# Performance work log

Measured on AMD Instinct MI355X. Metric: run time of the kernel, lower is better.

Reference implementation:

```python
import jax, jax.numpy as jnp
import numpy as np

D_IN, D_HID, D_CLS, N_CLASSES = 1024, 256, 128, 4
CELL_IN = 512
N = 50000


def setup_inputs() -> dict:
    key = jax.random.key(0)
    ks = jax.random.split(key, 20)
    s = 0.02
    inp = {
        "x_path": jax.random.normal(ks[0], (1, N, D_IN), jnp.float32),
        "x_cell": jax.random.normal(ks[1], (1, N, CELL_IN), jnp.float32),
        # wsi_net / cell_net projections
        "wsi_w": jax.random.normal(ks[2], (D_IN, D_HID), jnp.float32) * s,
        "wsi_b": jnp.zeros((D_HID,), jnp.float32),
        "cell_w": jax.random.normal(ks[3], (CELL_IN, D_HID), jnp.float32) * s,
        "cell_b": jnp.zeros((D_HID,), jnp.float32),
        # cross-attention Q/K/V
        "wq_w": jax.random.normal(ks[4], (D_HID, D_HID), jnp.float32) * s,
        "wq_b": jnp.zeros((D_HID,), jnp.float32),
        "wk_w": jax.random.normal(ks[5], (D_HID, D_HID), jnp.float32) * s,
        "wk_b": jnp.zeros((D_HID,), jnp.float32),
        "wv_w": jax.random.normal(ks[6], (D_HID, D_HID), jnp.float32) * s,
        "wv_b": jnp.zeros((D_HID,), jnp.float32),
        # gated attention (L=D=256, n_classes=1)
        "aa_w": jax.random.normal(ks[7], (D_HID, D_HID), jnp.float32) * s,
        "aa_b": jnp.zeros((D_HID,), jnp.float32),
        "ab_w": jax.random.normal(ks[8], (D_HID, D_HID), jnp.float32) * s,
        "ab_b": jnp.zeros((D_HID,), jnp.float32),
        "ac_w": jax.random.normal(ks[9], (D_HID, 1), jnp.float32) * s,
        "ac_b": jnp.zeros((1,), jnp.float32),
        # classifier MLP
        "c1_w": jax.random.normal(ks[10], (D_HID, D_CLS), jnp.float32) * s,
        "c1_b": jnp.zeros((D_CLS,), jnp.float32),
        "c2_w": jax.random.normal(ks[11], (D_CLS, N_CLASSES), jnp.float32) * s,
        "c2_b": jnp.zeros((N_CLASSES,), jnp.float32),
    }
    return inp


def reference(x_path, x_cell, wsi_w, wsi_b, cell_w, cell_b,
              wq_w, wq_b, wk_w, wk_b, wv_w, wv_b,
              aa_w, aa_b, ab_w, ab_b, ac_w, ac_b,
              c1_w, c1_b, c2_w, c2_b):
    xp = x_path[0]            # (N, D_IN)
    xc = x_cell[0]            # (N, CELL_IN)
    # instance-level projections (dropout inactive at eval)
    h_path = jax.nn.relu(xp @ wsi_w + wsi_b)    # (N, d)
    h_cell = jax.nn.relu(xc @ cell_w + cell_b)  # (N, d)
    # cross attention with per-instance seq_len=1 (bmm over N singleton batches)
    q = h_cell @ wq_w + wq_b
    k = h_path @ wk_w + wk_b
    v = h_path @ wv_w + wv_b
    scores = (jnp.einsum('nd,nd->n', q, k) / jnp.sqrt(jnp.float32(q.shape[-1])))[:, None, None]  # (N,1,1)
    attn_w = jax.nn.softmax(scores, axis=-1)     # (N,1,1), trivially ones
    fused = attn_w[:, 0, :] * v                  # (N, d)
    # gated attention MIL pooling
    a = jnp.tanh(fused @ aa_w + aa_b)
    b = jax.nn.sigmoid(fused @ ab_w + ab_b)
    A = (a * b) @ ac_w + ac_b                    # (N, 1)
    A_t = A.T                                    # (1, N)
    pooled = jax.nn.softmax(A_t, axis=1) @ fused # (1, d)
    # classifier MLP
    risk = jax.nn.relu(pooled @ c1_w + c1_b) @ c2_w + c2_b  # (1, n_classes)
    return risk
```

## Files before the change

kernel.cpp:

```cpp
#include <hip/hip_runtime.h>
#include <hip/hip_bf16.h>
#include <math.h>

#define D_IN 1024
#define D_HID 256
#define D_CLS 128
#define N_CLASSES 4
#define N_INST 50000

#define NPAD 50176
#define TILES 392
#define RG2 128
#define GB (NPAD / RG2)
#define PSTR 258
#define NEG_BIG (-1e30f)

#define ROWS 64
#define NBLK ((N_INST + ROWS - 1) / ROWS)
#define NB2 64
#define CHUNK ((NBLK + NB2 - 1) / NB2)

#define WS_W1T   0u
#define WS_WVT   524288u
#define WS_WAT   655360u
#define WS_WBT   786432u
#define WS_CNT   917504u
#define WS_P1    917760u
#define WS_XT    1322304u
#define WS_H     (WS_XT + 102760448u)
#define WS_NEED2 ((size_t)WS_H + 25690112u)
#define WS_P1F   917504u
#define WS_P2F   1724800u

typedef __attribute__((ext_vector_type(8))) short bf16x8;
typedef __attribute__((ext_vector_type(4))) float f32x4;

__device__ __forceinline__ short f2bf(float x) {
    __hip_bfloat16 h = __float2bfloat16(x);
    return *reinterpret_cast<short*>(&h);
}
__device__ __forceinline__ float fast_tanh(float x) {
    float e = __expf(2.f * x);
    return 1.f - 2.f * __builtin_amdgcn_rcpf(e + 1.f);
}
__device__ __forceinline__ float fast_sigmoid(float x) {
    return __builtin_amdgcn_rcpf(1.f + __expf(-x));
}
__device__ __forceinline__ bf16x8 cvt8(float4 a, float4 b) {
    bf16x8 r;
    r[0] = f2bf(a.x); r[1] = f2bf(a.y); r[2] = f2bf(a.z); r[3] = f2bf(a.w);
    r[4] = f2bf(b.x); r[5] = f2bf(b.y); r[6] = f2bf(b.z); r[7] = f2bf(b.w);
    return r;
}
__device__ __forceinline__ bf16x8 load_cvt8(const float* __restrict__ p) {
    return cvt8(*(const float4*)p, *(const float4*)(p + 4));
}

__global__ void convert_weights(const float* __restrict__ w1, const float* __restrict__ wv,
                                const float* __restrict__ wa, const float* __restrict__ wb,
                                __hip_bfloat16* __restrict__ w1t, __hip_bfloat16* __restrict__ wvt,
                                __hip_bfloat16* __restrict__ wat, __hip_bfloat16* __restrict__ wbt) {
    __shared__ __hip_bfloat16 T[64][68];
    int b = blockIdx.x, tid = threadIdx.x;
    const float* src; __hip_bfloat16* dst; int K, tr, tc;
    if (b < 64) { src = w1; dst = w1t; K = D_IN; tr = b >> 2; tc = b & 3; }
    else {
        int m = (b - 64) >> 4, t = (b - 64) & 15;
        src = (m == 0) ? wv : (m == 1) ? wa : wb;
        dst = (m == 0) ? wvt : (m == 1) ? wat : wbt;
        K = D_HID; tr = t >> 2; tc = t & 3;
    }
    int k0 = tr * 64, n0 = tc * 64;
#pragma unroll
    for (int p = 0; p < 4; p++) {
        int lin = p * 256 + tid;
        int r = lin >> 4;
        int c4 = (lin & 15) << 2;
        float4 v = *(const float4*)(src + (size_t)(k0 + r) * D_HID + n0 + c4);
        T[c4 + 0][r] = __float2bfloat16(v.x);
        T[c4 + 1][r] = __float2bfloat16(v.y);
        T[c4 + 2][r] = __float2bfloat16(v.z);
        T[c4 + 3][r] = __float2bfloat16(v.w);
    }
    __syncthreads();
#pragma unroll
    for (int p = 0; p < 4; p++) {
        int lin = p * 256 + tid;
        int n = lin >> 4;
        int kq = (lin & 15) << 2;
        ushort4 o;
        o.x = *(unsigned short*)&T[n][kq + 0];
        o.y = *(unsigned short*)&T[n][kq + 1];
        o.z = *(unsigned short*)&T[n][kq + 2];
        o.w = *(unsigned short*)&T[n][kq + 3];
        *(ushort4*)(dst + (size_t)(n0 + n) * K + k0 + kq) = o;
    }
}

__global__ __launch_bounds__(256, 2) void convert_xt(const float* __restrict__ xp,
                                                     __hip_bfloat16* __restrict__ xt) {
    __shared__ __hip_bfloat16 T[128][264];
    const int t = blockIdx.x >> 2;
    const int g = blockIdx.x & 3;
    const int tid = threadIdx.x;
    const int row = tid >> 1;
    const int half = tid & 1;
    const int row_g = t * 128 + row;
    const bool valid = row_g < N_INST;
    const float* src = xp + (size_t)row_g * D_IN + g * 256 + half * 128;
#pragma unroll 4
    for (int j = 0; j < 32; j++) {
        float4 v = {0.f, 0.f, 0.f, 0.f};
        if (valid) v = *(const float4*)(src + j * 4);
        int c = half * 128 + j * 4;
        ushort4 o;
        o.x = (unsigned short)f2bf(v.x);
        o.y = (unsigned short)f2bf(v.y);
        o.z = (unsigned short)f2bf(v.z);
        o.w = (unsigned short)f2bf(v.w);
        *(ushort4*)&T[row][c] = o;
    }
    __syncthreads();
#pragma unroll
    for (int i = 0; i < 16; i++) {
        int s = i * 256 + tid;
        int kg = s >> 7;
        int r2 = s & 127;
        bf16x8 v = *(const bf16x8*)&T[r2][kg * 8];
        int chunk = g * 8 + (kg >> 2);
        int quad = kg & 3;
        *(bf16x8*)(xt + (((size_t)(t * 32 + chunk) * 4 + quad) << 10) + r2 * 8) = v;
    }
}

__global__ __launch_bounds__(256, 2) void mcat_stage1(const __hip_bfloat16* __restrict__ xt,
                                                      const __hip_bfloat16* __restrict__ w1t,
                                                      const float* __restrict__ b1,
                                                      __hip_bfloat16* __restrict__ hout) {
    const int t    = blockIdx.x;
    const int tid  = threadIdx.x;
    const int wave = tid >> 6;
    const int lane = tid & 63;
    const int quad = lane >> 4;
    const int l16  = lane & 15;

    f32x4 acc[8][4];
    f32x4 zero = {0.f, 0.f, 0.f, 0.f};
#pragma unroll
    for (int i = 0; i < 8; i++)
#pragma unroll
        for (int j = 0; j < 4; j++) acc[i][j] = zero;

    const __hip_bfloat16* abase = xt + (size_t)t * 131072 + quad * 1024 + l16 * 8;
    const __hip_bfloat16* wbase[4];
#pragma unroll
    for (int ct = 0; ct < 4; ct++)
        wbase[ct] = w1t + (size_t)(wave * 64 + ct * 16 + l16) * D_IN + quad * 8;

#pragma unroll 4
    for (int kc = 0; kc < 32; kc++) {
        bf16x8 af[8];
#pragma unroll
        for (int rt = 0; rt < 8; rt++)
            af[rt] = *(const bf16x8*)(abase + kc * 4096 + rt * 128);
        bf16x8 bf[4];
#pragma unroll
        for (int ct = 0; ct < 4; ct++)
            bf[ct] = *(const bf16x8*)(wbase[ct] + kc * 32);
#pragma unroll
        for (int ct = 0; ct < 4; ct++)
#pragma unroll
            for (int rt = 0; rt < 8; rt++)
                acc[rt][ct] = __builtin_amdgcn_mfma_f32_16x16x32_bf16(af[rt], bf[ct], acc[rt][ct], 0, 0, 0);
    }

#pragma unroll
    for (int ct = 0; ct < 4; ct++) {
        const int col = wave * 64 + ct * 16 + l16;
        const float bias = b1[col];
        __hip_bfloat16* hb = hout + (((size_t)(t * 8 + (col >> 5)) * 4 + ((col >> 3) & 3)) << 10) + (col & 7);
#pragma unroll
        for (int rt = 0; rt < 8; rt++)
#pragma unroll
            for (int r = 0; r < 4; r++) {
                int row = rt * 16 + quad * 4 + r;
                hb[row * 8] = __float2bfloat16(fmaxf(acc[rt][ct][r] + bias, 0.f));
            }
    }
}

__global__ __launch_bounds__(512, 1) void mcat_stage2(const __hip_bfloat16* __restrict__ h,
                          const __hip_bfloat16* __restrict__ wvt, const float* __restrict__ bv,
                          const __hip_bfloat16* __restrict__ wat, const float* __restrict__ ba,
                          const __hip_bfloat16* __restrict__ wbt, const float* __restrict__ bb,
                          const float* __restrict__ acw, const float* __restrict__ acb,
                          float* __restrict__ p1, unsigned int* __restrict__ counter,
                          const float* __restrict__ c1w, const float* __restrict__ c1b,
                          const float* __restrict__ c2w, const float* __restrict__ c2b,
                          float* __restrict__ out) {
    __shared__ __hip_bfloat16 Vs[RG2][264];
    __shared__ float Apart[8][RG2];
    __shared__ float ExpW[RG2];
    __shared__ float smx[4];
    __shared__ float scb[GB];
    __shared__ float pooled[D_HID];
    __shared__ float r1v[D_CLS];

    const int tid  = threadIdx.x;
    const int wave = tid >> 6;
    const int lane = tid & 63;
    const int quad = lane >> 4;
    const int l16  = lane & 15;
    const int cb   = wave * 32;
    const int row0 = blockIdx.x * RG2;

    f32x4 acc[8][2];
    f32x4 zero = {0.f, 0.f, 0.f, 0.f};

    const __hip_bfloat16* hb = h + (size_t)blockIdx.x * 32768 + quad * 1024 + l16 * 8;
#pragma unroll
    for (int i = 0; i < 8; i++) { acc[i][0] = zero; acc[i][1] = zero; }
    {
        const __hip_bfloat16* w0 = wvt + (size_t)(cb + l16) * D_HID + quad * 8;
        const __hip_bfloat16* w1p = w0 + 16 * D_HID;
#pragma unroll
        for (int ks = 0; ks < 8; ks++) {
            bf16x8 b0 = *(const bf16x8*)(w0 + ks * 32);
            bf16x8 b1f = *(const bf16x8*)(w1p + ks * 32);
#pragma unroll
            for (int rt = 0; rt < 8; rt++) {
                bf16x8 af = *(const bf16x8*)(hb + ks * 4096 + rt * 128);
                acc[rt][0] = __builtin_amdgcn_mfma_f32_16x16x32_bf16(af, b0, acc[rt][0], 0, 0, 0);
                acc[rt][1] = __builtin_amdgcn_mfma_f32_16x16x32_bf16(af, b1f, acc[rt][1], 0, 0, 0);
            }
        }
    }
#pragma unroll
    for (int ct = 0; ct < 2; ct++) {
        int col = cb + ct * 16 + l16;
        float bias = bv[col];
#pragma unroll
        for (int rt = 0; rt < 8; rt++)
#pragma unroll
            for (int r = 0; r < 4; r++)
                Vs[rt * 16 + quad * 4 + r][col] = __float2bfloat16(acc[rt][ct][r] + bias);
    }
    __syncthreads();

    float a_reg[8][2][4];
#pragma unroll
    for (int i = 0; i < 8; i++) { acc[i][0] = zero; acc[i][1] = zero; }
    {
        const __hip_bfloat16* w0 = wat + (size_t)(cb + l16) * D_HID + quad * 8;
        const __hip_bfloat16* w1p = w0 + 16 * D_HID;
#pragma unroll
        for (int ks = 0; ks < 8; ks++) {
            bf16x8 b0 = *(const bf16x8*)(w0 + ks * 32);
            bf16x8 b1f = *(const bf16x8*)(w1p + ks * 32);
#pragma unroll
            for (int rt = 0; rt < 8; rt++) {
                bf16x8 af = *(const bf16x8*)&Vs[rt * 16 + l16][ks * 32 + quad * 8];
                acc[rt][0] = __builtin_amdgcn_mfma_f32_16x16x32_bf16(af, b0, acc[rt][0], 0, 0, 0);
                acc[rt][1] = __builtin_amdgcn_mfma_f32_16x16x32_bf16(af, b1f, acc[rt][1], 0, 0, 0);
            }
        }
    }
#pragma unroll
    for (int ct = 0; ct < 2; ct++) {
        float bias = ba[cb + ct * 16 + l16];
#pragma unroll
        for (int rt = 0; rt < 8; rt++)
#pragma unroll
            for (int r = 0; r < 4; r++)
                a_reg[rt][ct][r] = fast_tanh(acc[rt][ct][r] + bias);
    }

#pragma unroll
    for (int i = 0; i < 8; i++) { acc[i][0] = zero; acc[i][1] = zero; }
    {
        const __hip_bfloat16* w0 = wbt + (size_t)(cb + l16) * D_HID + quad * 8;
        const __hip_bfloat16* w1p = w0 + 16 * D_HID;
#pragma unroll
        for (int ks = 0; ks < 8; ks++) {
            bf16x8 b0 = *(const bf16x8*)(w0 + ks * 32);
            bf16x8 b1f = *(const bf16x8*)(w1p + ks * 32);
#pragma unroll
            for (int rt = 0; rt < 8; rt++) {
                bf16x8 af = *(const bf16x8*)&Vs[rt * 16 + l16][ks * 32 + quad * 8];
                acc[rt][0] = __builtin_amdgcn_mfma_f32_16x16x32_bf16(af, b0, acc[rt][0], 0, 0, 0);
                acc[rt][1] = __builtin_amdgcn_mfma_f32_16x16x32_bf16(af, b1f, acc[rt][1], 0, 0, 0);
            }
        }
    }
    {
        float acw0 = acw[cb + l16], acw1 = acw[cb + 16 + l16];
        float bb0 = bb[cb + l16],  bb1 = bb[cb + 16 + l16];
        float sp[8][4];
#pragma unroll
        for (int rt = 0; rt < 8; rt++)
#pragma unroll
            for (int r = 0; r < 4; r++) {
                float g0 = a_reg[rt][0][r] * fast_sigmoid(acc[rt][0][r] + bb0);
                float g1 = a_reg[rt][1][r] * fast_sigmoid(acc[rt][1][r] + bb1);
                sp[rt][r] = g0 * acw0 + g1 * acw1;
            }
#pragma unroll
        for (int off = 1; off < 16; off <<= 1)
#pragma unroll
            for (int rt = 0; rt < 8; rt++)
#pragma unroll
                for (int r = 0; r < 4; r++)
                    sp[rt][r] += __shfl_xor(sp[rt][r], off, 16);
        if (l16 == 0) {
#pragma unroll
            for (int rt = 0; rt < 8; rt++)
#pragma unroll
                for (int r = 0; r < 4; r++)
                    Apart[wave][rt * 16 + quad * 4 + r] = sp[rt][r];
        }
    }
    __syncthreads();

    if (tid < 64) {
        float A0 = acb[0], A1 = acb[0];
#pragma unroll
        for (int w = 0; w < 8; w++) { A0 += Apart[w][tid]; A1 += Apart[w][tid + 64]; }
        bool v0 = (row0 + tid) < N_INST;
        bool v1 = (row0 + 64 + tid) < N_INST;
        if (!v0) A0 = NEG_BIG;
        if (!v1) A1 = NEG_BIG;
        float m = fmaxf(A0, A1);
#pragma unroll
        for (int off = 32; off > 0; off >>= 1) m = fmaxf(m, __shfl_xor(m, off));
        float e0 = v0 ? __expf(A0 - m) : 0.f;
        float e1 = v1 ? __expf(A1 - m) : 0.f;
        ExpW[tid] = e0; ExpW[tid + 64] = e1;
        float ssum = e0 + e1;
#pragma unroll
        for (int off = 32; off > 0; off >>= 1) ssum += __shfl_xor(ssum, off);
        if (tid == 0) {
            p1[(size_t)blockIdx.x * PSTR + 0] = m;
            p1[(size_t)blockIdx.x * PSTR + 1] = ssum;
        }
    }
    __syncthreads();
    if (tid < 256) {
        float p = 0.f;
#pragma unroll 8
        for (int n = 0; n < RG2; n++)
            p += ExpW[n] * __bfloat162float(Vs[n][tid]);
        p1[(size_t)blockIdx.x * PSTR + 2 + tid] = p;
    }

    __syncthreads();
    if (tid == 0) {
        __threadfence();
        unsigned int old = __hip_atomic_fetch_add(counter, 1u, __ATOMIC_ACQ_REL, __HIP_MEMORY_SCOPE_AGENT);
        smx[3] = (old == GB - 1) ? 1.f : 0.f;
    }
    __syncthreads();
    if (smx[3] == 0.f) return;
    __threadfence();

    {
        float mloc = NEG_BIG;
        for (int b = tid; b < GB; b += 512) mloc = fmaxf(mloc, p1[(size_t)b * PSTR]);
#pragma unroll
        for (int off = 32; off > 0; off >>= 1) mloc = fmaxf(mloc, __shfl_xor(mloc, off));
        if (lane == 0) ExpW[wave] = mloc;
    }
    __syncthreads();
    if (tid == 0) {
        float M = NEG_BIG;
#pragma unroll
        for (int w = 0; w < 8; w++) M = fmaxf(M, ExpW[w]);
        smx[0] = M;
    }
    __syncthreads();
    {
        float M = smx[0];
        float sl = 0.f;
        for (int b = tid; b < GB; b += 512) {
            float s = __expf(p1[(size_t)b * PSTR] - M);
            scb[b] = s;
            sl += s * p1[(size_t)b * PSTR + 1];
        }
#pragma unroll
        for (int off = 32; off > 0; off >>= 1) sl += __shfl_xor(sl, off);
        if (lane == 0) ExpW[8 + wave] = sl;
    }
    __syncthreads();
    if (tid == 0) {
        float S = 0.f;
#pragma unroll
        for (int w = 0; w < 8; w++) S += ExpW[8 + w];
        smx[1] = S;
    }
    __syncthreads();
    if (tid < 256) {
        float p = 0.f;
        for (int b = 0; b < GB; b++)
            p += scb[b] * p1[(size_t)b * PSTR + 2 + tid];
        pooled[tid] = p / smx[1];
    }
    __syncthreads();
    if (tid < D_CLS) {
        float a2 = c1b[tid];
#pragma unroll 8
        for (int d = 0; d < D_HID; d++)
            a2 += pooled[d] * c1w[(size_t)d * D_CLS + tid];
        r1v[tid] = fmaxf(a2, 0.f);
    }
    __syncthreads();
    if (tid < N_CLASSES) {
        float a2 = c2b[tid];
#pragma unroll 8
        for (int j = 0; j < D_CLS; j++)
            a2 += r1v[j] * c2w[(size_t)j * N_CLASSES + tid];
        out[tid] = a2;
    }
}

__device__ __forceinline__ void gemm256_w8(const __hip_bfloat16 (*S)[264],
                                           const __hip_bfloat16* __restrict__ Wt,
                                           int colbase, int quad, int l16, f32x4 acc[4][2]) {
    f32x4 zero = {0.f, 0.f, 0.f, 0.f};
#pragma unroll
    for (int i = 0; i < 4; i++) { acc[i][0] = zero; acc[i][1] = zero; }
    const __hip_bfloat16* w0 = Wt + (size_t)(colbase + l16) * D_HID + quad * 8;
    const __hip_bfloat16* w1 = w0 + 16 * D_HID;
#pragma unroll
    for (int ks = 0; ks < 8; ks++) {
        bf16x8 af[4];
#pragma unroll
        for (int rt = 0; rt < 4; rt++)
            af[rt] = *(const bf16x8*)&S[rt * 16 + l16][ks * 32 + quad * 8];
        bf16x8 b0 = *(const bf16x8*)(w0 + ks * 32);
        bf16x8 b1 = *(const bf16x8*)(w1 + ks * 32);
#pragma unroll
        for (int rt = 0; rt < 4; rt++) {
            acc[rt][0] = __builtin_amdgcn_mfma_f32_16x16x32_bf16(af[rt], b0, acc[rt][0], 0, 0, 0);
            acc[rt][1] = __builtin_amdgcn_mfma_f32_16x16x32_bf16(af[rt], b1, acc[rt][1], 0, 0, 0);
        }
    }
}

__global__ __launch_bounds__(512, 4) void mcat_mainF(const float* __restrict__ xsrc,
                          const __hip_bfloat16* __restrict__ w1t, const float* __restrict__ b1,
                          const __hip_bfloat16* __restrict__ wvt, const float* __restrict__ bv,
                          const __hip_bfloat16* __restrict__ wat, const float* __restrict__ ba,
                          const __hip_bfloat16* __restrict__ wbt, const float* __restrict__ bb,
                          const float* __restrict__ acw, const float* __restrict__ acb,
                          float* __restrict__ partials) {
    __shared__ __hip_bfloat16 Hs[ROWS][264];
    __shared__ __hip_bfloat16 Vs[ROWS][264];
    __shared__ float Apart[8][ROWS];
    __shared__ float ExpW[ROWS];
    const int tid  = threadIdx.x;
    const int wave = tid >> 6;
    const int lane = tid & 63;
    const int quad = lane >> 4;
    const int l16  = lane & 15;
    const int colbase = wave * 32;
    const int row0 = blockIdx.x * ROWS;
    f32x4 acc[4][2];
    f32x4 zero = {0.f, 0.f, 0.f, 0.f};
#pragma unroll
    for (int i = 0; i < 4; i++) { acc[i][0] = zero; acc[i][1] = zero; }
    const float* xf_base[4];
#pragma unroll
    for (int rt = 0; rt < 4; rt++) {
        int r = row0 + rt * 16 + l16;
        if (r > N_INST - 1) r = N_INST - 1;
        xf_base[rt] = xsrc + (size_t)r * D_IN + quad * 8;
    }
    const __hip_bfloat16* wb0 = w1t + (size_t)(colbase + l16) * D_IN + quad * 8;
    const __hip_bfloat16* wb1 = wb0 + 16 * D_IN;
    for (int kc = 0; kc < D_IN; kc += 32) {
        bf16x8 af[4];
#pragma unroll
        for (int rt = 0; rt < 4; rt++) af[rt] = load_cvt8(xf_base[rt] + kc);
        bf16x8 b0 = *(const bf16x8*)(wb0 + kc);
        bf16x8 b1 = *(const bf16x8*)(wb1 + kc);
#pragma unroll
        for (int rt = 0; rt < 4; rt++) {
            acc[rt][0] = __builtin_amdgcn_mfma_f32_16x16x32_bf16(af[rt], b0, acc[rt][0], 0, 0, 0);
            acc[rt][1] = __builtin_amdgcn_mfma_f32_16x16x32_bf16(af[rt], b1, acc[rt][1], 0, 0, 0);
        }
    }
#pragma unroll
    for (int ct = 0; ct < 2; ct++) {
        int col = colbase + ct * 16 + l16;
        float bias = b1[col];
#pragma unroll
        for (int rt = 0; rt < 4; rt++)
#pragma unroll
            for (int r = 0; r < 4; r++)
                Hs[rt * 16 + quad * 4 + r][col] = __float2bfloat16(fmaxf(acc[rt][ct][r] + bias, 0.f));
    }
    __syncthreads();
    gemm256_w8(Hs, wvt, colbase, quad, l16, acc);
#pragma unroll
    for (int ct = 0; ct < 2; ct++) {
        int col = colbase + ct * 16 + l16;
        float bias = bv[col];
#pragma unroll
        for (int rt = 0; rt < 4; rt++)
#pragma unroll
            for (int r = 0; r < 4; r++)
                Vs[rt * 16 + quad * 4 + r][col] = __float2bfloat16(acc[rt][ct][r] + bias);
    }
    __syncthreads();
    float a_reg[4][2][4];
    gemm256_w8(Vs, wat, colbase, quad, l16, acc);
#pragma unroll
    for (int ct = 0; ct < 2; ct++) {
        float bias = ba[colbase + ct * 16 + l16];
#pragma unroll
        for (int rt = 0; rt < 4; rt++)
#pragma unroll
            for (int r = 0; r < 4; r++)
                a_reg[rt][ct][r] = fast_tanh(acc[rt][ct][r] + bias);
    }
    gemm256_w8(Vs, wbt, colbase, quad, l16, acc);
    {
        float acw0 = acw[colbase + l16];
        float acw1 = acw[colbase + 16 + l16];
        float bias0 = bb[colbase + l16];
        float bias1 = bb[colbase + 16 + l16];
        float sp[4][4];
#pragma unroll
        for (int rt = 0; rt < 4; rt++)
#pragma unroll
            for (int r = 0; r < 4; r++) {
                float g0 = a_reg[rt][0][r] * fast_sigmoid(acc[rt][0][r] + bias0);
                float g1 = a_reg[rt][1][r] * fast_sigmoid(acc[rt][1][r] + bias1);
                sp[rt][r] = g0 * acw0 + g1 * acw1;
            }
#pragma unroll
        for (int off = 1; off < 16; off <<= 1)
#pragma unroll
            for (int rt = 0; rt < 4; rt++)
#pragma unroll
                for (int r = 0; r < 4; r++)
                    sp[rt][r] += __shfl_xor(sp[rt][r], off, 16);
        if (l16 == 0) {
#pragma unroll
            for (int rt = 0; rt < 4; rt++)
#pragma unroll
                for (int r = 0; r < 4; r++)
                    Apart[wave][rt * 16 + quad * 4 + r] = sp[rt][r];
        }
    }
    __syncthreads();
    if (tid < 64) {
        bool valid = (row0 + tid) < N_INST;
        float A = acb[0];
#pragma unroll
        for (int w = 0; w < 8; w++) A += Apart[w][tid];
        if (!valid) A = NEG_BIG;
        float m = A;
#pragma unroll
        for (int off = 32; off > 0; off >>= 1) m = fmaxf(m, __shfl_xor(m, off));
        float e = valid ? __expf(A - m) : 0.f;
        ExpW[tid] = e;
        float ssum = e;
#pragma unroll
        for (int off = 32; off > 0; off >>= 1) ssum += __shfl_xor(ssum, off);
        if (tid == 0) {
            partials[(size_t)blockIdx.x * PSTR + 0] = m;
            partials[(size_t)blockIdx.x * PSTR + 1] = ssum;
        }
    }
    __syncthreads();
    if (tid < 256) {
        float p = 0.f;
#pragma unroll 8
        for (int n = 0; n < 64; n++)
            p += ExpW[n] * __bfloat162float(Vs[n][tid]);
        partials[(size_t)blockIdx.x * PSTR + 2 + tid] = p;
    }
}

__global__ void mcat_fin_a(const float* __restrict__ p1, float* __restrict__ p2) {
    __shared__ float sm[1];
    int g = blockIdx.x, tid = threadIdx.x;
    int lo = g * CHUNK;
    int hi = lo + CHUNK; if (hi > NBLK) hi = NBLK;
    if (tid < 64) {
        float m = NEG_BIG;
        if (lo + tid < hi) m = p1[(size_t)(lo + tid) * PSTR];
#pragma unroll
        for (int off = 32; off > 0; off >>= 1) m = fmaxf(m, __shfl_xor(m, off));
        if (tid == 0) sm[0] = m;
    }
    __syncthreads();
    float M = sm[0];
    float p = 0.f, sacc = 0.f;
    for (int b = lo; b < hi; b++) {
        float sc = __expf(p1[(size_t)b * PSTR] - M);
        sacc += sc * p1[(size_t)b * PSTR + 1];
        p += sc * p1[(size_t)b * PSTR + 2 + tid];
    }
    if (tid == 0) {
        p2[(size_t)g * PSTR + 0] = M;
        p2[(size_t)g * PSTR + 1] = sacc;
    }
    p2[(size_t)g * PSTR + 2 + tid] = p;
}

__global__ void mcat_fin_b(const float* __restrict__ p2,
                           const float* __restrict__ c1w, const float* __restrict__ c1b,
                           const float* __restrict__ c2w, const float* __restrict__ c2b,
                           float* __restrict__ out) {
    __shared__ float sm[2];
    __shared__ float sc[NB2];
    __shared__ float pooled[D_HID];
    __shared__ float r1[D_CLS];
    int tid = threadIdx.x;
    if (tid < 64) {
        float m = p2[(size_t)tid * PSTR];
#pragma unroll
        for (int off = 32; off > 0; off >>= 1) m = fmaxf(m, __shfl_xor(m, off));
        if (tid == 0) sm[0] = m;
    }
    __syncthreads();
    float M = sm[0];
    if (tid < 64) {
        float s = __expf(p2[(size_t)tid * PSTR] - M);
        sc[tid] = s;
        float Ssum = s * p2[(size_t)tid * PSTR + 1];
#pragma unroll
        for (int off = 32; off > 0; off >>= 1) Ssum += __shfl_xor(Ssum, off);
        if (tid == 0) sm[1] = Ssum;
    }
    __syncthreads();
    float S = sm[1];
    float p = 0.f;
#pragma unroll 8
    for (int b = 0; b < NB2; b++)
        p += sc[b] * p2[(size_t)b * PSTR + 2 + tid];
    pooled[tid] = p / S;
    __syncthreads();
    if (tid < D_CLS) {
        float acc = c1b[tid];
#pragma unroll 8
        for (int d = 0; d < D_HID; d++)
            acc += pooled[d] * c1w[(size_t)d * D_CLS + tid];
        r1[tid] = fmaxf(acc, 0.f);
    }
    __syncthreads();
    if (tid < N_CLASSES) {
        float acc = c2b[tid];
#pragma unroll 8
        for (int j = 0; j < D_CLS; j++)
            acc += r1[j] * c2w[(size_t)j * N_CLASSES + tid];
        out[tid] = acc;
    }
}

extern "C" void kernel_launch(void* const* d_in, const int* in_sizes, int n_in,
                              void* d_out, int out_size, void* d_ws, size_t ws_size,
                              hipStream_t stream) {
    const float* xp  = (const float*)d_in[0];
    const float* w1  = (const float*)d_in[2];
    const float* b1  = (const float*)d_in[3];
    const float* wv  = (const float*)d_in[10];
    const float* bv  = (const float*)d_in[11];
    const float* wa  = (const float*)d_in[12];
    const float* ba  = (const float*)d_in[13];
    const float* wb  = (const float*)d_in[14];
    const float* bb  = (const float*)d_in[15];
    const float* acw = (const float*)d_in[16];
    const float* acb = (const float*)d_in[17];
    const float* c1w = (const float*)d_in[18];
    const float* c1b = (const float*)d_in[19];
    const float* c2w = (const float*)d_in[20];
    const float* c2b = (const float*)d_in[21];
    float* out = (float*)d_out;

    char* ws = (char*)d_ws;
    __hip_bfloat16* w1t = (__hip_bfloat16*)(ws + WS_W1T);
    __hip_bfloat16* wvt = (__hip_bfloat16*)(ws + WS_WVT);
    __hip_bfloat16* wat = (__hip_bfloat16*)(ws + WS_WAT);
    __hip_bfloat16* wbt = (__hip_bfloat16*)(ws + WS_WBT);

    hipLaunchKernelGGL(convert_weights, dim3(112), dim3(256), 0, stream,
                       w1, wv, wa, wb, w1t, wvt, wat, wbt);

    if (ws_size >= WS_NEED2) {
        unsigned int* counter = (unsigned int*)(ws + WS_CNT);
        float* p1 = (float*)(ws + WS_P1);
        __hip_bfloat16* xt = (__hip_bfloat16*)(ws + WS_XT);
        __hip_bfloat16* h  = (__hip_bfloat16*)(ws + WS_H);
        hipMemsetAsync(counter, 0, 4, stream);
        hipLaunchKernelGGL(convert_xt, dim3(TILES * 4), dim3(256), 0, stream, xp, xt);
        hipLaunchKernelGGL(mcat_stage1, dim3(TILES), dim3(256), 0, stream, xt, w1t, b1, h);
        hipLaunchKernelGGL(mcat_stage2, dim3(GB), dim3(512), 0, stream,
                           h, wvt, bv, wat, ba, wbt, bb, acw, acb, p1, counter,
                           c1w, c1b, c2w, c2b, out);
    } else {
        float* p1 = (float*)(ws + WS_P1F);
        float* p2 = (float*)(ws + WS_P2F);
        hipLaunchKernelGGL(mcat_mainF, dim3(NBLK), dim3(512), 0, stream,
                           xp, w1t, b1, wvt, bv, wat, ba, wbt, bb, acw, acb, p1);
        hipLaunchKernelGGL(mcat_fin_a, dim3(NB2), dim3(256), 0, stream, p1, p2);
        hipLaunchKernelGGL(mcat_fin_b, dim3(1), dim3(256), 0, stream,
                           p2, c1w, c1b, c2w, c2b, out);
    }
}
```

Baseline: 628.3 us.

## Fuse fp32-to-bf16 conversion of x_path into the stage-1 GEMM with LDS double buffering

Removes the separate convert_xt kernel, which wrote a bf16 pre-tiled copy of x_path to workspace that stage 1 then read back. The new stage-1 kernel loads fp32 rows directly, converts them to bf16 into a double-buffered LDS tile, and prefetches the next K chunk while MFMAs run on the current one. Tiles shrink from 128 to 64 rows to allow three blocks per CU. This avoids a large intermediate write and read plus a kernel launch, but adds per-chunk block barriers and smaller tiles, so each tile reuses the weights less.

```diff
diff --git a/kernel.cpp b/kernel.cpp
--- a/kernel.cpp
+++ b/kernel.cpp
@@ -9,7 +9,7 @@
 #define N_INST 50000
 
 #define NPAD 50176
-#define TILES 392
+#define G1 (NPAD / 64)
 #define RG2 128
 #define GB (NPAD / RG2)
 #define PSTR 258
@@ -26,8 +26,7 @@
 #define WS_WBT   786432u
 #define WS_CNT   917504u
 #define WS_P1    917760u
-#define WS_XT    1322304u
-#define WS_H     (WS_XT + 102760448u)
+#define WS_H     1322304u
 #define WS_NEED2 ((size_t)WS_H + 25690112u)
 #define WS_P1F   917504u
 #define WS_P2F   1724800u
@@ -45,6 +44,14 @@
 }
 __device__ __forceinline__ float fast_sigmoid(float x) {
     return __builtin_amdgcn_rcpf(1.f + __expf(-x));
+}
+__device__ __forceinline__ ushort4 cvt4u(float4 a) {
+    ushort4 o;
+    o.x = (unsigned short)f2bf(a.x);
+    o.y = (unsigned short)f2bf(a.y);
+    o.z = (unsigned short)f2bf(a.z);
+    o.w = (unsigned short)f2bf(a.w);
+    return o;
 }
 __device__ __forceinline__ bf16x8 cvt8(float4 a, float4 b) {
     bf16x8 r;
@@ -97,90 +104,89 @@
     }
 }
 
-__global__ __launch_bounds__(256, 2) void convert_xt(const float* __restrict__ xp,
-                                                     __hip_bfloat16* __restrict__ xt) {
-    __shared__ __hip_bfloat16 T[128][264];
-    const int t = blockIdx.x >> 2;
-    const int g = blockIdx.x & 3;
-    const int tid = threadIdx.x;
-    const int row = tid >> 1;
-    const int half = tid & 1;
-    const int row_g = t * 128 + row;
-    const bool valid = row_g < N_INST;
-    const float* src = xp + (size_t)row_g * D_IN + g * 256 + half * 128;
-#pragma unroll 4
-    for (int j = 0; j < 32; j++) {
-        float4 v = {0.f, 0.f, 0.f, 0.f};
-        if (valid) v = *(const float4*)(src + j * 4);
-        int c = half * 128 + j * 4;
-        ushort4 o;
-        o.x = (unsigned short)f2bf(v.x);
-        o.y = (unsigned short)f2bf(v.y);
-        o.z = (unsigned short)f2bf(v.z);
-        o.w = (unsigned short)f2bf(v.w);
-        *(ushort4*)&T[row][c] = o;
-    }
-    __syncthreads();
-#pragma unroll
-    for (int i = 0; i < 16; i++) {
-        int s = i * 256 + tid;
-        int kg = s >> 7;
-        int r2 = s & 127;
-        bf16x8 v = *(const bf16x8*)&T[r2][kg * 8];
-        int chunk = g * 8 + (kg >> 2);
-        int quad = kg & 3;
-        *(bf16x8*)(xt + (((size_t)(t * 32 + chunk) * 4 + quad) << 10) + r2 * 8) = v;
-    }
-}
-
-__global__ __launch_bounds__(256, 2) void mcat_stage1(const __hip_bfloat16* __restrict__ xt,
-                                                      const __hip_bfloat16* __restrict__ w1t,
-                                                      const float* __restrict__ b1,
-                                                      __hip_bfloat16* __restrict__ hout) {
-    const int t    = blockIdx.x;
+__global__ __launch_bounds__(256, 3) void mcat_stage1f(const float* __restrict__ xp,
+                                                       const __hip_bfloat16* __restrict__ w1t,
+                                                       const float* __restrict__ b1,
+                                                       __hip_bfloat16* __restrict__ hout) {
+    __shared__ __hip_bfloat16 Xs[2][64][72];
     const int tid  = threadIdx.x;
     const int wave = tid >> 6;
     const int lane = tid & 63;
     const int quad = lane >> 4;
     const int l16  = lane & 15;
-
-    f32x4 acc[8][4];
+    const int row0 = blockIdx.x * 64;
+    const int t128 = blockIdx.x >> 1;
+    const int rhalf = blockIdx.x & 1;
+
+    const int srow = tid >> 4;
+    const int sc4  = (tid & 15) << 2;
+    const float* xsrc[4];
+#pragma unroll
+    for (int p = 0; p < 4; p++) {
+        int rg = row0 + p * 16 + srow;
+        if (rg > N_INST - 1) rg = N_INST - 1;
+        xsrc[p] = xp + (size_t)rg * D_IN + sc4;
+    }
+
+    f32x4 acc[4][4];
     f32x4 zero = {0.f, 0.f, 0.f, 0.f};
 #pragma unroll
-    for (int i = 0; i < 8; i++)
+    for (int i = 0; i < 4; i++)
 #pragma unroll
         for (int j = 0; j < 4; j++) acc[i][j] = zero;
 
-    const __hip_bfloat16* abase = xt + (size_t)t * 131072 + quad * 1024 + l16 * 8;
     const __hip_bfloat16* wbase[4];
 #pragma unroll
     for (int ct = 0; ct < 4; ct++)
         wbase[ct] = w1t + (size_t)(wave * 64 + ct * 16 + l16) * D_IN + quad * 8;
 
-#pragma unroll 4
-    for (int kc = 0; kc < 32; kc++) {
-        bf16x8 af[8];
-#pragma unroll
-        for (int rt = 0; rt < 8; rt++)
-            af[rt] = *(const bf16x8*)(abase + kc * 4096 + rt * 128);
-        bf16x8 bf[4];
-#pragma unroll
-        for (int ct = 0; ct < 4; ct++)
-            bf[ct] = *(const bf16x8*)(wbase[ct] + kc * 32);
-#pragma unroll
-        for (int ct = 0; ct < 4; ct++)
-#pragma unroll
-            for (int rt = 0; rt < 8; rt++)
-                acc[rt][ct] = __builtin_amdgcn_mfma_f32_16x16x32_bf16(af[rt], bf[ct], acc[rt][ct], 0, 0, 0);
+    float4 ld[4];
+#pragma unroll
+    for (int p = 0; p < 4; p++) ld[p] = *(const float4*)(xsrc[p]);
+#pragma unroll
+    for (int p = 0; p < 4; p++)
+        *(ushort4*)&Xs[0][p * 16 + srow][sc4] = cvt4u(ld[p]);
+    __syncthreads();
+
+    for (int kc = 0; kc < 16; kc++) {
+        const int buf = kc & 1;
+        if (kc < 15) {
+#pragma unroll
+            for (int p = 0; p < 4; p++)
+                ld[p] = *(const float4*)(xsrc[p] + (kc + 1) * 64);
+        }
+#pragma unroll
+        for (int ks = 0; ks < 2; ks++) {
+            bf16x8 af[4];
+#pragma unroll
+            for (int rt = 0; rt < 4; rt++)
+                af[rt] = *(const bf16x8*)&Xs[buf][rt * 16 + l16][ks * 32 + quad * 8];
+            bf16x8 bfv[4];
+#pragma unroll
+            for (int ct = 0; ct < 4; ct++)
+                bfv[ct] = *(const bf16x8*)(wbase[ct] + kc * 64 + ks * 32);
+#pragma unroll
+            for (int ct = 0; ct < 4; ct++)
+#pragma unroll
+                for (int rt = 0; rt < 4; rt++)
+                    acc[rt][ct] = __builtin_amdgcn_mfma_f32_16x16x32_bf16(af[rt], bfv[ct], acc[rt][ct], 0, 0, 0);
+        }
+        if (kc < 15) {
+#pragma unroll
+            for (int p = 0; p < 4; p++)
+                *(ushort4*)&Xs[buf ^ 1][p * 16 + srow][sc4] = cvt4u(ld[p]);
+        }
+        __syncthreads();
     }
 
 #pragma unroll
     for (int ct = 0; ct < 4; ct++) {
         const int col = wave * 64 + ct * 16 + l16;
         const float bias = b1[col];
-        __hip_bfloat16* hb = hout + (((size_t)(t * 8 + (col >> 5)) * 4 + ((col >> 3) & 3)) << 10) + (col & 7);
-#pragma unroll
-        for (int rt = 0; rt < 8; rt++)
+        __hip_bfloat16* hb = hout + (((size_t)(t128 * 8 + (col >> 5)) * 4 + ((col >> 3) & 3)) << 10)
+                                  + rhalf * 512 + (col & 7);
+#pragma unroll
+        for (int rt = 0; rt < 4; rt++)
 #pragma unroll
             for (int r = 0; r < 4; r++) {
                 int row = rt * 16 + quad * 4 + r;
@@ -691,11 +697,9 @@
     if (ws_size >= WS_NEED2) {
         unsigned int* counter = (unsigned int*)(ws + WS_CNT);
         float* p1 = (float*)(ws + WS_P1);
-        __hip_bfloat16* xt = (__hip_bfloat16*)(ws + WS_XT);
         __hip_bfloat16* h  = (__hip_bfloat16*)(ws + WS_H);
         hipMemsetAsync(counter, 0, 4, stream);
-        hipLaunchKernelGGL(convert_xt, dim3(TILES * 4), dim3(256), 0, stream, xp, xt);
-        hipLaunchKernelGGL(mcat_stage1, dim3(TILES), dim3(256), 0, stream, xt, w1t, b1, h);
+        hipLaunchKernelGGL(mcat_stage1f, dim3(G1), dim3(256), 0, stream, xp, w1t, b1, h);
         hipLaunchKernelGGL(mcat_stage2, dim3(GB), dim3(512), 0, stream,
                            h, wvt, bv, wat, ba, wbt, bb, acw, acb, p1, counter,
                            c1w, c1b, c2w, c2b, out);
```

Result: faster. 536.1 us (-14.7%).
